# Kernel tuning notes

Measured on AMD Instinct MI355X. Metric: run time of the kernel, lower is better.

## Reference

```python
import jax, jax.numpy as jnp
import numpy as np

T = 2048
HIDDEN = 4096
NQ = 32
NKV = 8
HD = 128
THETA = 10000.0


def setup_inputs() -> dict:
    key = jax.random.key(0)
    ks = jax.random.split(key, 5)
    s = 1.0 / np.sqrt(HIDDEN)
    return {
        "positions": jnp.arange(T, dtype=jnp.int32),
        "hidden_states": jax.random.normal(ks[0], (T, HIDDEN), dtype=jnp.float32),
        "wq": jax.random.normal(ks[1], (HIDDEN, NQ * HD), dtype=jnp.float32) * s,
        "wk": jax.random.normal(ks[2], (HIDDEN, NKV * HD), dtype=jnp.float32) * s,
        "wv": jax.random.normal(ks[3], (HIDDEN, NKV * HD), dtype=jnp.float32) * s,
        "wo": jax.random.normal(ks[4], (NQ * HD, HIDDEN), dtype=jnp.float32) * s,
    }


def _rope_neox(x, positions):
    # x: [T, H, HD]; neox style: split halves, rotate
    half = HD // 2
    inv_freq = 1.0 / (THETA ** (jnp.arange(0, half, dtype=jnp.float32) / half))
    ang = positions.astype(jnp.float32)[:, None] * inv_freq[None, :]  # [T, half]
    cos = jnp.cos(ang)[:, None, :]  # [T, 1, half]
    sin = jnp.sin(ang)[:, None, :]
    x1, x2 = x[..., :half], x[..., half:]
    return jnp.concatenate([x1 * cos - x2 * sin, x2 * cos + x1 * sin], axis=-1)


def reference(positions, hidden_states, wq, wk, wv, wo):
    scale = HD ** -0.5
    q = (hidden_states @ wq).reshape(T, NQ, HD)
    k = (hidden_states @ wk).reshape(T, NKV, HD)
    v = (hidden_states @ wv).reshape(T, NKV, HD)
    q = _rope_neox(q, positions)
    k = _rope_neox(k, positions)
    # GQA: repeat kv heads to match q heads
    group = NQ // NKV
    k_r = jnp.repeat(k, group, axis=1)  # [T, NQ, HD]
    v_r = jnp.repeat(v, group, axis=1)
    scores = jnp.einsum('qhd,khd->hqk', q, k_r) * scale  # [NQ, T, T]
    causal = positions[:, None] >= positions[None, :]  # [T, T]
    scores = jnp.where(causal[None, :, :], scores, -jnp.inf)
    probs = jax.nn.softmax(scores, axis=-1)
    attn = jnp.einsum('hqk,khd->qhd', probs, v_r).reshape(T, NQ * HD)
    return attn @ wo
```

## Files before the change

kernel.cpp:

```cpp
#include <hip/hip_runtime.h>

#define T_SEQ  2048
#define HID    4096
#define NQH    32
#define NKVH   8
#define HDIM   128

typedef float  f32x4  __attribute__((ext_vector_type(4)));
typedef __bf16 bf16x8 __attribute__((ext_vector_type(8)));
typedef __bf16 bf16x4 __attribute__((ext_vector_type(4)));

__device__ __forceinline__ float bf2f(unsigned short u) {
  union { unsigned int i; float f; } v; v.i = ((unsigned int)u) << 16; return v.f;
}
__device__ __forceinline__ unsigned short f2bf(float f) {
  union { float f; unsigned int i; } v; v.f = f;
  unsigned int r = v.i + 0x7fffu + ((v.i >> 16) & 1u);
  return (unsigned short)(r >> 16);
}

__device__ __forceinline__ f32x4 mfma_bf16(bf16x8 a, bf16x8 b, f32x4 c) {
  return __builtin_amdgcn_mfma_f32_16x16x32_bf16(a, b, c, 0, 0, 0);
}

#define GLOAD16(g, l)                                              \
  __builtin_amdgcn_global_load_lds(                                \
      (const __attribute__((address_space(1))) void*)(g),          \
      (__attribute__((address_space(3))) void*)(l), 16, 0, 0)

__global__ void prep_qw(const float* __restrict__ hs, unsigned short* __restrict__ hb,
                        const float* __restrict__ wq, unsigned short* __restrict__ wt) {
  __shared__ float tile[64][65];
  if (blockIdx.x < 8192) {
    long long i = ((long long)blockIdx.x * 256 + threadIdx.x) * 4;
    float4 v = *(const float4*)(hs + i);
    union { unsigned short u[4]; uint2 p; } o;
    o.u[0] = f2bf(v.x); o.u[1] = f2bf(v.y); o.u[2] = f2bf(v.z); o.u[3] = f2bf(v.w);
    *(uint2*)(hb + i) = o.p;
    return;
  }
  const int bid = blockIdx.x - 8192;
  const int N = NQH * HDIM, K = HID;
  int n0 = (bid & 63) * 64, k0 = (bid >> 6) * 64;
  int tx = threadIdx.x & 15, ty = threadIdx.x >> 4;
#pragma unroll
  for (int i = 0; i < 4; i++) {
    int k = ty + 16 * i;
    float4 f = *(const float4*)(wq + (long long)(k0 + k) * N + n0 + tx * 4);
    tile[tx * 4 + 0][k] = f.x;
    tile[tx * 4 + 1][k] = f.y;
    tile[tx * 4 + 2][k] = f.z;
    tile[tx * 4 + 3][k] = f.w;
  }
  __syncthreads();
#pragma unroll
  for (int i = 0; i < 4; i++) {
    int n = ty + 16 * i;
    union { unsigned short u[4]; uint2 p; } o;
    o.u[0] = f2bf(tile[n][tx * 4 + 0]);
    o.u[1] = f2bf(tile[n][tx * 4 + 1]);
    o.u[2] = f2bf(tile[n][tx * 4 + 2]);
    o.u[3] = f2bf(tile[n][tx * 4 + 3]);
    *(uint2*)(wt + (long long)(n0 + n) * K + k0 + tx * 4) = o.p;
  }
}

__global__ void transpose_conv(const float* __restrict__ W,
                               unsigned short* __restrict__ Wt, int K, int N) {
  __shared__ float tile[64][65];
  int n0 = blockIdx.x * 64, k0 = blockIdx.y * 64;
  int tx = threadIdx.x & 15, ty = threadIdx.x >> 4;
#pragma unroll
  for (int i = 0; i < 4; i++) {
    int k = ty + 16 * i;
    float4 f = *(const float4*)(W + (long long)(k0 + k) * N + n0 + tx * 4);
    tile[tx * 4 + 0][k] = f.x;
    tile[tx * 4 + 1][k] = f.y;
    tile[tx * 4 + 2][k] = f.z;
    tile[tx * 4 + 3][k] = f.w;
  }
  __syncthreads();
#pragma unroll
  for (int i = 0; i < 4; i++) {
    int n = ty + 16 * i;
    union { unsigned short u[4]; uint2 p; } o;
    o.u[0] = f2bf(tile[n][tx * 4 + 0]);
    o.u[1] = f2bf(tile[n][tx * 4 + 1]);
    o.u[2] = f2bf(tile[n][tx * 4 + 2]);
    o.u[3] = f2bf(tile[n][tx * 4 + 3]);
    *(uint2*)(Wt + (long long)(n0 + n) * K + k0 + tx * 4) = o.p;
  }
}

__global__ void transpose_conv_kv(const float* __restrict__ Wk,
                                  const float* __restrict__ Wv,
                                  unsigned short* __restrict__ Wt) {
  __shared__ float tile[64][65];
  const int N = NKVH * HDIM, K = HID;
  const float* W = blockIdx.z ? Wv : Wk;
  unsigned short* dst = Wt + (size_t)blockIdx.z * N * K;
  int n0 = blockIdx.x * 64, k0 = blockIdx.y * 64;
  int tx = threadIdx.x & 15, ty = threadIdx.x >> 4;
#pragma unroll
  for (int i = 0; i < 4; i++) {
    int k = ty + 16 * i;
    float4 f = *(const float4*)(W + (long long)(k0 + k) * N + n0 + tx * 4);
    tile[tx * 4 + 0][k] = f.x;
    tile[tx * 4 + 1][k] = f.y;
    tile[tx * 4 + 2][k] = f.z;
    tile[tx * 4 + 3][k] = f.w;
  }
  __syncthreads();
#pragma unroll
  for (int i = 0; i < 4; i++) {
    int n = ty + 16 * i;
    union { unsigned short u[4]; uint2 p; } o;
    o.u[0] = f2bf(tile[n][tx * 4 + 0]);
    o.u[1] = f2bf(tile[n][tx * 4 + 1]);
    o.u[2] = f2bf(tile[n][tx * 4 + 2]);
    o.u[3] = f2bf(tile[n][tx * 4 + 3]);
    *(uint2*)(dst + (long long)(n0 + n) * K + k0 + tx * 4) = o.p;
  }
}

template <int EPI>
__global__ __launch_bounds__(256) void gemm_bt(const unsigned short* __restrict__ A,
                                               const unsigned short* __restrict__ Bt,
                                               void* __restrict__ Cv,
                                               int M, int N, int K) {
  __shared__ unsigned short As[128 * 64];
  __shared__ unsigned short Bs[128 * 64];
  const int lin = blockIdx.y * gridDim.x + blockIdx.x;
  const int cpx = (gridDim.x * gridDim.y) >> 3;
  const int swz = (lin & 7) * cpx + (lin >> 3);
  const int bx = swz % gridDim.x, by = swz / gridDim.x;

  const int t = threadIdx.x;
  const int lane = t & 63, w = t >> 6;
  const int wr = w >> 1, wc = w & 1;
  const int l15 = lane & 15, lg = lane >> 4;
  const int m0 = by * 128, n0 = bx * 128;

  f32x4 acc[4][4];
#pragma unroll
  for (int i = 0; i < 4; i++)
#pragma unroll
    for (int j = 0; j < 4; j++) acc[i][j] = (f32x4){0.f, 0.f, 0.f, 0.f};

  for (int kt = 0; kt < K; kt += 64) {
    __syncthreads();
#pragma unroll
    for (int s = 0; s < 4; s++) {
      int c = t + s * 256;
      int row = c >> 3, sub = c & 7;
      GLOAD16(A + (long long)(m0 + row) * K + kt + ((sub ^ (row & 7)) * 8),
              (char*)As + (w * 64 + s * 256) * 16);
      GLOAD16(Bt + (long long)(n0 + row) * K + kt + ((sub ^ (row & 7)) * 8),
              (char*)Bs + (w * 64 + s * 256) * 16);
    }
    __syncthreads();

#pragma unroll
    for (int kk = 0; kk < 2; kk++) {
      bf16x8 af[4], bfr[4];
#pragma unroll
      for (int mi = 0; mi < 4; mi++) {
        int row = wr * 64 + mi * 16 + l15;
        af[mi] = *(const bf16x8*)(As + row * 64 + (((kk * 4 + lg) ^ (row & 7)) * 8));
      }
#pragma unroll
      for (int ni = 0; ni < 4; ni++) {
        int row = wc * 64 + ni * 16 + l15;
        bfr[ni] = *(const bf16x8*)(Bs + row * 64 + (((kk * 4 + lg) ^ (row & 7)) * 8));
      }
#pragma unroll
      for (int mi = 0; mi < 4; mi++)
#pragma unroll
        for (int ni = 0; ni < 4; ni++)
          acc[mi][ni] = mfma_bf16(af[mi], bfr[ni], acc[mi][ni]);
    }
  }

  const int row0 = m0 + wr * 64, col0 = n0 + wc * 64;
#pragma unroll
  for (int mi = 0; mi < 4; mi++)
#pragma unroll
    for (int ni = 0; ni < 4; ni++) {
      int rbase = row0 + mi * 16 + lg * 4;
      int col = col0 + ni * 16 + l15;
#pragma unroll
      for (int r = 0; r < 4; r++) {
        float v = acc[mi][ni][r];
        if (EPI == 0)
          ((unsigned short*)Cv)[(long long)(rbase + r) * N + col] = f2bf(v);
        else
          ((float*)Cv)[(long long)(rbase + r) * N + col] = v;
      }
    }
}

__global__ __launch_bounds__(256) void gemm_kv64(const unsigned short* __restrict__ A,
                                                 const unsigned short* __restrict__ Bt,
                                                 unsigned short* __restrict__ Ckv,
                                                 unsigned short* __restrict__ Cvt) {
  __shared__ unsigned short As[64 * 64];
  __shared__ unsigned short Bs[128 * 64];
  __shared__ unsigned short Tt[128 * 64];
  const int lin = blockIdx.y * gridDim.x + blockIdx.x;
  const int swz = (lin & 7) * 64 + (lin >> 3);
  const int bx = swz & 15, by = swz >> 4;

  const int t = threadIdx.x;
  const int lane = t & 63, w = t >> 6;
  const int wr = w >> 1, wc = w & 1;
  const int l15 = lane & 15, lg = lane >> 4;
  const int m0 = by * 64, n0 = bx * 128;
  const int K = HID;

  f32x4 acc[2][4];
#pragma unroll
  for (int i = 0; i < 2; i++)
#pragma unroll
    for (int j = 0; j < 4; j++) acc[i][j] = (f32x4){0.f, 0.f, 0.f, 0.f};

  for (int kt = 0; kt < K; kt += 64) {
    __syncthreads();
#pragma unroll
    for (int s = 0; s < 2; s++) {
      int c = t + s * 256;
      int row = c >> 3, sub = c & 7;
      GLOAD16(A + (long long)(m0 + row) * K + kt + ((sub ^ (row & 7)) * 8),
              (char*)As + (w * 64 + s * 256) * 16);
    }
#pragma unroll
    for (int s = 0; s < 4; s++) {
      int c = t + s * 256;
      int row = c >> 3, sub = c & 7;
      GLOAD16(Bt + (long long)(n0 + row) * K + kt + ((sub ^ (row & 7)) * 8),
              (char*)Bs + (w * 64 + s * 256) * 16);
    }
    __syncthreads();

#pragma unroll
    for (int kk = 0; kk < 2; kk++) {
      bf16x8 af[2], bfr[4];
#pragma unroll
      for (int mi = 0; mi < 2; mi++) {
        int row = wr * 32 + mi * 16 + l15;
        af[mi] = *(const bf16x8*)(As + row * 64 + (((kk * 4 + lg) ^ (row & 7)) * 8));
      }
#pragma unroll
      for (int ni = 0; ni < 4; ni++) {
        int row = wc * 64 + ni * 16 + l15;
        bfr[ni] = *(const bf16x8*)(Bs + row * 64 + (((kk * 4 + lg) ^ (row & 7)) * 8));
      }
#pragma unroll
      for (int mi = 0; mi < 2; mi++)
#pragma unroll
        for (int ni = 0; ni < 4; ni++)
          acc[mi][ni] = mfma_bf16(af[mi], bfr[ni], acc[mi][ni]);
    }
  }

  const int row0 = m0 + wr * 32, col0 = n0 + wc * 64;
  if (n0 < 1024) {
#pragma unroll
    for (int mi = 0; mi < 2; mi++)
#pragma unroll
      for (int ni = 0; ni < 4; ni++) {
        int rbase = row0 + mi * 16 + lg * 4;
        int col = col0 + ni * 16 + l15;
#pragma unroll
        for (int r = 0; r < 4; r++)
          Ckv[(long long)(rbase + r) * 1024 + col] = f2bf(acc[mi][ni][r]);
      }
  } else {
#pragma unroll
    for (int mi = 0; mi < 2; mi++)
#pragma unroll
      for (int ni = 0; ni < 4; ni++) {
        int nloc = wc * 64 + ni * 16 + l15;
#pragma unroll
        for (int r = 0; r < 4; r++) {
          int mloc = wr * 32 + mi * 16 + lg * 4 + r;
          Tt[nloc * 64 + (mloc ^ ((nloc & 7) << 3))] = f2bf(acc[mi][ni][r]);
        }
      }
    __syncthreads();
    const int nloc = t >> 1;
#pragma unroll
    for (int cc = 0; cc < 4; cc++) {
      int ci = (t & 1) * 4 + cc;
      int sc = ci ^ (nloc & 7);
      uint4 v = *(const uint4*)(Tt + nloc * 64 + sc * 8);
      *(uint4*)(Cvt + (long long)(n0 - 1024 + nloc) * T_SEQ + m0 + ci * 8) = v;
    }
  }
}

__global__ void rope_all(unsigned short* __restrict__ qb,
                         unsigned short* __restrict__ kb,
                         const int* __restrict__ positions) {
  const int w = threadIdx.x >> 6, d = threadIdx.x & 63;
  const int gid = blockIdx.x * 4 + w;
  unsigned short* row;
  int t;
  bool isq;
  if (gid < T_SEQ * NQH) {
    int h = gid & (NQH - 1); t = gid >> 5;
    row = qb + (size_t)t * (NQH * HDIM) + (size_t)h * HDIM;
    isq = true;
  } else {
    int g = gid - T_SEQ * NQH;
    int h = g & (NKVH - 1); t = g >> 3;
    row = kb + (size_t)t * (NKVH * HDIM) + (size_t)h * HDIM;
    isq = false;
  }
  double inv = exp2(-(double)d * 0.20762050593046014);
  double ang = (double)positions[t] * inv;
  double c = cos(ang), s = sin(ang);
  if (isq) { c *= 0.12751744416986895; s *= 0.12751744416986895; }
  float x1 = bf2f(row[d]), x2 = bf2f(row[d + 64]);
  row[d]      = f2bf((float)((double)x1 * c - (double)x2 * s));
  row[d + 64] = f2bf((float)((double)x2 * c + (double)x1 * s));
}

__global__ __launch_bounds__(256) void attn_kernel(const unsigned short* __restrict__ qb,
                                                   const unsigned short* __restrict__ kb,
                                                   const unsigned short* __restrict__ vt,
                                                   unsigned short* __restrict__ ab) {
  __shared__ unsigned short Ks[64 * 128];
  __shared__ unsigned short Vs[128 * 64];

  const int lin = blockIdx.y * gridDim.x + blockIdx.x;
  const int swz = (lin & 7) * 128 + (lin >> 3);
  const int bx = swz & 63;
  const int hp = swz >> 6;
  const int kvh = hp >> 1;
  const int t = threadIdx.x, lane = t & 63, w = t >> 6;
  const int l15 = lane & 15, lg = lane >> 4;
  const int head = 2 * hp + (w & 1);
  const int wr16 = (w >> 1) * 16;
  const int jt = (hp & 1) ? bx : 63 - bx;
  const int q0 = jt * 32;

  bf16x8 qf[4];
#pragma unroll
  for (int kk = 0; kk < 4; kk++)
    qf[kk] = *(const bf16x8*)(qb + (long long)(q0 + wr16 + l15) * (NQH * HDIM) +
                              head * HDIM + kk * 32 + lg * 8);

  f32x4 accO[8];
#pragma unroll
  for (int db = 0; db < 8; db++) accO[db] = (f32x4){0.f, 0.f, 0.f, 0.f};
  float mrun = -3e38f, lrun = 0.f;

  const int jd = jt >> 1;
  for (int kt = 0; kt <= jd; kt++) {
    __syncthreads();
#pragma unroll
    for (int s = 0; s < 4; s++) {
      int c = t + s * 256;
      int row = c >> 4, chk = c & 15;
      GLOAD16(kb + (long long)(kt * 64 + row) * (NKVH * HDIM) + kvh * HDIM +
                  ((chk ^ (row & 7)) * 8),
              (char*)Ks + (w * 64 + s * 256) * 16);
    }
#pragma unroll
    for (int s = 0; s < 4; s++) {
      int c = t + s * 256;
      int row = c >> 3, chk = c & 7;
      GLOAD16(vt + (long long)(kvh * HDIM + row) * T_SEQ + kt * 64 +
                  ((chk ^ (row & 7)) * 8),
              (char*)Vs + (w * 64 + s * 256) * 16);
    }
    __syncthreads();

    f32x4 accS[4];
#pragma unroll
    for (int kc = 0; kc < 4; kc++) accS[kc] = (f32x4){0.f, 0.f, 0.f, 0.f};
    __builtin_amdgcn_s_setprio(1);
#pragma unroll
    for (int kk = 0; kk < 4; kk++)
#pragma unroll
      for (int kc = 0; kc < 4; kc++) {
        int row = kc * 16 + l15;
        bf16x8 a = *(const bf16x8*)(Ks + row * 128 + (((kk * 4 + lg) ^ (l15 & 7)) * 8));
        accS[kc] = mfma_bf16(a, qf[kk], accS[kc]);
      }
    __builtin_amdgcn_s_setprio(0);

    float pm[4][4];
    if (kt == jd) {
      const int qloc = (jt & 1) * 32 + wr16 + l15;
#pragma unroll
      for (int kc = 0; kc < 4; kc++)
#pragma unroll
        for (int r = 0; r < 4; r++)
          pm[kc][r] = (kc * 16 + lg * 4 + r > qloc) ? -3e38f : accS[kc][r];
    } else {
#pragma unroll
      for (int kc = 0; kc < 4; kc++)
#pragma unroll
        for (int r = 0; r < 4; r++) pm[kc][r] = accS[kc][r];
    }

    float rm = pm[0][0];
#pragma unroll
    for (int kc = 0; kc < 4; kc++)
#pragma unroll
      for (int r = 0; r < 4; r++) rm = fmaxf(rm, pm[kc][r]);
    if (__any(rm > mrun + 8.f)) {
      rm = fmaxf(rm, __shfl_xor(rm, 16, 64));
      rm = fmaxf(rm, __shfl_xor(rm, 32, 64));
      float mn = fmaxf(mrun, rm);
      float corr = exp2f(mrun - mn);
      mrun = mn;
      lrun *= corr;
      float cO[4];
#pragma unroll
      for (int r = 0; r < 4; r++) cO[r] = __shfl(corr, lg * 4 + r, 64);
#pragma unroll
      for (int db = 0; db < 8; db++)
#pragma unroll
        for (int r = 0; r < 4; r++) accO[db][r] *= cO[r];
    }

    float p[4][4];
#pragma unroll
    for (int kc = 0; kc < 4; kc++)
#pragma unroll
      for (int r = 0; r < 4; r++) {
        p[kc][r] = exp2f(pm[kc][r] - mrun);
        lrun += p[kc][r];
      }
    bf16x8 pa0, pa1;
#pragma unroll
    for (int j = 0; j < 8; j++) {
      pa0[j] = (__bf16)p[(j >> 2)][j & 3];
      pa1[j] = (__bf16)p[2 + (j >> 2)][j & 3];
    }

    const int swl = l15 & 7;
    const int coff = (lg & 1) * 4;
    const int c80 = lg >> 1;
    __builtin_amdgcn_s_setprio(1);
#pragma unroll
    for (int db = 0; db < 8; db++) {
      int vb = (db * 16 + l15) * 64;
      union { bf16x8 v; bf16x4 h[2]; } b;
      b.h[0] = *(const bf16x4*)(Vs + vb + ((c80 ^ swl) * 8 + coff));
      b.h[1] = *(const bf16x4*)(Vs + vb + (((c80 + 2) ^ swl) * 8 + coff));
      accO[db] = mfma_bf16(pa0, b.v, accO[db]);
    }
#pragma unroll
    for (int db = 0; db < 8; db++) {
      int vb = (db * 16 + l15) * 64;
      union { bf16x8 v; bf16x4 h[2]; } b;
      b.h[0] = *(const bf16x4*)(Vs + vb + (((c80 + 4) ^ swl) * 8 + coff));
      b.h[1] = *(const bf16x4*)(Vs + vb + (((c80 + 6) ^ swl) * 8 + coff));
      accO[db] = mfma_bf16(pa1, b.v, accO[db]);
    }
    __builtin_amdgcn_s_setprio(0);
  }

  lrun += __shfl_xor(lrun, 16, 64);
  lrun += __shfl_xor(lrun, 32, 64);
  float lO[4];
#pragma unroll
  for (int r = 0; r < 4; r++) lO[r] = __shfl(lrun, lg * 4 + r, 64);
#pragma unroll
  for (int db = 0; db < 8; db++)
#pragma unroll
    for (int r = 0; r < 4; r++) {
      int qr = q0 + wr16 + lg * 4 + r;
      int col = head * HDIM + db * 16 + l15;
      ((__bf16*)ab)[(long long)qr * (NQH * HDIM) + col] = (__bf16)(accO[db][r] / lO[r]);
    }
}

extern "C" void kernel_launch(void* const* d_in, const int* in_sizes, int n_in,
                              void* d_out, int out_size, void* d_ws, size_t ws_size,
                              hipStream_t stream) {
  const int*   positions = (const int*)d_in[0];
  const float* hs = (const float*)d_in[1];
  const float* wq = (const float*)d_in[2];
  const float* wk = (const float*)d_in[3];
  const float* wv = (const float*)d_in[4];
  const float* wo = (const float*)d_in[5];
  float* out = (float*)d_out;

  const size_t SZ_WT = (size_t)HID * HID * 2;
  const size_t SZ_HB = (size_t)T_SEQ * HID * 2;
  const size_t SZ_QB = (size_t)T_SEQ * NQH * HDIM * 2;
  const size_t SZ_KB = (size_t)T_SEQ * NKVH * HDIM * 2;
  const size_t need = SZ_WT + SZ_HB + SZ_QB + SZ_KB * 2;
  if (ws_size < need) return;

  char* p = (char*)d_ws;
  unsigned short* wt  = (unsigned short*)p; p += SZ_WT;
  unsigned short* hb  = (unsigned short*)p; p += SZ_HB;
  unsigned short* qb  = (unsigned short*)p; p += SZ_QB;
  unsigned short* kb  = (unsigned short*)p; p += SZ_KB;
  unsigned short* vtb = (unsigned short*)p; p += SZ_KB;
  unsigned short* ab  = hb;

  prep_qw<<<8192 + 4096, 256, 0, stream>>>(hs, hb, wq, wt);
  gemm_bt<0><<<dim3((NQH * HDIM) / 128, T_SEQ / 128), 256, 0, stream>>>(hb, wt, qb, T_SEQ, NQH * HDIM, HID);

  transpose_conv_kv<<<dim3((NKVH * HDIM) / 64, HID / 64, 2), 256, 0, stream>>>(wk, wv, wt);
  gemm_kv64<<<dim3(16, 32), 256, 0, stream>>>(hb, wt, kb, vtb);

  rope_all<<<(T_SEQ * (NQH + NKVH)) / 4, 256, 0, stream>>>(qb, kb, positions);

  attn_kernel<<<dim3(64, 16), 256, 0, stream>>>(qb, kb, vtb, ab);

  transpose_conv<<<dim3(HID / 64, (NQH * HDIM) / 64), 256, 0, stream>>>(wo, wt, NQH * HDIM, HID);
  gemm_bt<2><<<dim3(HID / 128, T_SEQ / 128), 256, 0, stream>>>(ab, wt, out, T_SEQ, HID, NQH * HDIM);
}
```

Measured before the change: 390.5 us.

## Make attention a persistent kernel with per-XCD atomic work queues

Replaces the fixed 64x16 attention grid with 512 persistent blocks. Each block pulls work items (one head, one 64-row query tile) from a per-XCD atomic counter, which rope_all resets. Items are handed out longest-first and each XCD is pinned to one KV head, to improve load balance and L2 reuse of K/V. The V^T store in gemm_kv64 is reordered so the attention kernel can read V fragments as single 16-byte LDS loads instead of two 8-byte halves. The risks are atomic overhead, a dependence on round-robin mapping of blocks to XCDs, and fewer blocks in flight.

```diff
diff --git a/kernel.cpp b/kernel.cpp
--- a/kernel.cpp
+++ b/kernel.cpp
@@ -8,7 +8,6 @@
 
 typedef float  f32x4  __attribute__((ext_vector_type(4)));
 typedef __bf16 bf16x8 __attribute__((ext_vector_type(8)));
-typedef __bf16 bf16x4 __attribute__((ext_vector_type(4)));
 
 __device__ __forceinline__ float bf2f(unsigned short u) {
   union { unsigned int i; float f; } v; v.i = ((unsigned int)u) << 16; return v.f;
@@ -289,18 +288,21 @@
     __syncthreads();
     const int nloc = t >> 1;
 #pragma unroll
-    for (int cc = 0; cc < 4; cc++) {
-      int ci = (t & 1) * 4 + cc;
-      int sc = ci ^ (nloc & 7);
-      uint4 v = *(const uint4*)(Tt + nloc * 64 + sc * 8);
-      *(uint4*)(Cvt + (long long)(n0 - 1024 + nloc) * T_SEQ + m0 + ci * 8) = v;
+    for (int cc = 0; cc < 8; cc++) {
+      int ci = (t & 1) * 8 + cc;
+      uint2 v = *(const uint2*)(Tt + nloc * 64 +
+                                (((ci >> 1) ^ (nloc & 7)) * 8 + (ci & 1) * 4));
+      int nc = (ci >> 3) * 8 + 2 * (ci & 3) + ((ci >> 2) & 1);
+      *(uint2*)(Cvt + (long long)(n0 - 1024 + nloc) * T_SEQ + m0 + nc * 4) = v;
     }
   }
 }
 
 __global__ void rope_all(unsigned short* __restrict__ qb,
                          unsigned short* __restrict__ kb,
-                         const int* __restrict__ positions) {
+                         const int* __restrict__ positions,
+                         int* __restrict__ cnt) {
+  if (blockIdx.x == 0 && threadIdx.x < 8) cnt[threadIdx.x] = 0;
   const int w = threadIdx.x >> 6, d = threadIdx.x & 63;
   const int gid = blockIdx.x * 4 + w;
   unsigned short* row;
@@ -328,155 +330,153 @@
 __global__ __launch_bounds__(256) void attn_kernel(const unsigned short* __restrict__ qb,
                                                    const unsigned short* __restrict__ kb,
                                                    const unsigned short* __restrict__ vt,
-                                                   unsigned short* __restrict__ ab) {
+                                                   unsigned short* __restrict__ ab,
+                                                   int* __restrict__ cnt) {
   __shared__ unsigned short Ks[64 * 128];
   __shared__ unsigned short Vs[128 * 64];
-
-  const int lin = blockIdx.y * gridDim.x + blockIdx.x;
-  const int swz = (lin & 7) * 128 + (lin >> 3);
-  const int bx = swz & 63;
-  const int hp = swz >> 6;
-  const int kvh = hp >> 1;
+  __shared__ int s_item;
+
+  const int xcd = blockIdx.x & 7;
+  const int kvh = xcd;
   const int t = threadIdx.x, lane = t & 63, w = t >> 6;
   const int l15 = lane & 15, lg = lane >> 4;
-  const int head = 2 * hp + (w & 1);
-  const int wr16 = (w >> 1) * 16;
-  const int jt = (hp & 1) ? bx : 63 - bx;
-  const int q0 = jt * 32;
-
-  bf16x8 qf[4];
-#pragma unroll
-  for (int kk = 0; kk < 4; kk++)
-    qf[kk] = *(const bf16x8*)(qb + (long long)(q0 + wr16 + l15) * (NQH * HDIM) +
-                              head * HDIM + kk * 32 + lg * 8);
-
-  f32x4 accO[8];
-#pragma unroll
-  for (int db = 0; db < 8; db++) accO[db] = (f32x4){0.f, 0.f, 0.f, 0.f};
-  float mrun = -3e38f, lrun = 0.f;
-
-  const int jd = jt >> 1;
-  for (int kt = 0; kt <= jd; kt++) {
-    __syncthreads();
-#pragma unroll
-    for (int s = 0; s < 4; s++) {
-      int c = t + s * 256;
-      int row = c >> 4, chk = c & 15;
-      GLOAD16(kb + (long long)(kt * 64 + row) * (NKVH * HDIM) + kvh * HDIM +
-                  ((chk ^ (row & 7)) * 8),
-              (char*)Ks + (w * 64 + s * 256) * 16);
-    }
-#pragma unroll
-    for (int s = 0; s < 4; s++) {
-      int c = t + s * 256;
-      int row = c >> 3, chk = c & 7;
-      GLOAD16(vt + (long long)(kvh * HDIM + row) * T_SEQ + kt * 64 +
-                  ((chk ^ (row & 7)) * 8),
-              (char*)Vs + (w * 64 + s * 256) * 16);
-    }
-    __syncthreads();
-
-    f32x4 accS[4];
-#pragma unroll
-    for (int kc = 0; kc < 4; kc++) accS[kc] = (f32x4){0.f, 0.f, 0.f, 0.f};
-    __builtin_amdgcn_s_setprio(1);
+
+  for (;;) {
+    __syncthreads();
+    if (t == 0) s_item = atomicAdd(&cnt[xcd], 1);
+    __syncthreads();
+    const int item = s_item;
+    if (item >= 128) break;
+    const int j = 31 - (item >> 2);
+    const int head = xcd * 4 + (item & 3);
+    const int q0 = j * 64;
+
+    bf16x8 qf[4];
 #pragma unroll
     for (int kk = 0; kk < 4; kk++)
-#pragma unroll
-      for (int kc = 0; kc < 4; kc++) {
-        int row = kc * 16 + l15;
-        bf16x8 a = *(const bf16x8*)(Ks + row * 128 + (((kk * 4 + lg) ^ (l15 & 7)) * 8));
-        accS[kc] = mfma_bf16(a, qf[kk], accS[kc]);
-      }
-    __builtin_amdgcn_s_setprio(0);
-
-    float pm[4][4];
-    if (kt == jd) {
-      const int qloc = (jt & 1) * 32 + wr16 + l15;
+      qf[kk] = *(const bf16x8*)(qb + (long long)(q0 + w * 16 + l15) * (NQH * HDIM) +
+                                head * HDIM + kk * 32 + lg * 8);
+
+    f32x4 accO[8];
+#pragma unroll
+    for (int db = 0; db < 8; db++) accO[db] = (f32x4){0.f, 0.f, 0.f, 0.f};
+    float mrun = -3e38f, lrun = 0.f;
+
+    for (int kt = 0; kt <= j; kt++) {
+      __syncthreads();
+#pragma unroll
+      for (int s = 0; s < 4; s++) {
+        int c = t + s * 256;
+        int row = c >> 4, chk = c & 15;
+        GLOAD16(kb + (long long)(kt * 64 + row) * (NKVH * HDIM) + kvh * HDIM +
+                    ((chk ^ (row & 7)) * 8),
+                (char*)Ks + (w * 64 + s * 256) * 16);
+      }
+#pragma unroll
+      for (int s = 0; s < 4; s++) {
+        int c = t + s * 256;
+        int row = c >> 3, chk = c & 7;
+        GLOAD16(vt + (long long)(kvh * HDIM + row) * T_SEQ + kt * 64 +
+                    ((chk ^ (row & 7)) * 8),
+                (char*)Vs + (w * 64 + s * 256) * 16);
+      }
+      __syncthreads();
+
+      f32x4 accS[4];
+#pragma unroll
+      for (int kc = 0; kc < 4; kc++) accS[kc] = (f32x4){0.f, 0.f, 0.f, 0.f};
+      __builtin_amdgcn_s_setprio(1);
+#pragma unroll
+      for (int kk = 0; kk < 4; kk++)
+#pragma unroll
+        for (int kc = 0; kc < 4; kc++) {
+          int row = kc * 16 + l15;
+          bf16x8 a = *(const bf16x8*)(Ks + row * 128 + (((kk * 4 + lg) ^ (l15 & 7)) * 8));
+          accS[kc] = mfma_bf16(a, qf[kk], accS[kc]);
+        }
+      __builtin_amdgcn_s_setprio(0);
+
+      float pm[4][4];
+      if (kt == j) {
+        const int qloc = w * 16 + l15;
+#pragma unroll
+        for (int kc = 0; kc < 4; kc++)
+#pragma unroll
+          for (int r = 0; r < 4; r++)
+            pm[kc][r] = (kc * 16 + lg * 4 + r > qloc) ? -3e38f : accS[kc][r];
+      } else {
+#pragma unroll
+        for (int kc = 0; kc < 4; kc++)
+#pragma unroll
+          for (int r = 0; r < 4; r++) pm[kc][r] = accS[kc][r];
+      }
+
+      float rm = pm[0][0];
 #pragma unroll
       for (int kc = 0; kc < 4; kc++)
 #pragma unroll
-        for (int r = 0; r < 4; r++)
-          pm[kc][r] = (kc * 16 + lg * 4 + r > qloc) ? -3e38f : accS[kc][r];
-    } else {
+        for (int r = 0; r < 4; r++) rm = fmaxf(rm, pm[kc][r]);
+      if (__any(rm > mrun + 8.f)) {
+        rm = fmaxf(rm, __shfl_xor(rm, 16, 64));
+        rm = fmaxf(rm, __shfl_xor(rm, 32, 64));
+        float mn = fmaxf(mrun, rm);
+        float corr = exp2f(mrun - mn);
+        mrun = mn;
+        lrun *= corr;
+        float cO[4];
+#pragma unroll
+        for (int r = 0; r < 4; r++) cO[r] = __shfl(corr, lg * 4 + r, 64);
+#pragma unroll
+        for (int db = 0; db < 8; db++)
+#pragma unroll
+          for (int r = 0; r < 4; r++) accO[db][r] *= cO[r];
+      }
+
+      float p[4][4];
 #pragma unroll
       for (int kc = 0; kc < 4; kc++)
 #pragma unroll
-        for (int r = 0; r < 4; r++) pm[kc][r] = accS[kc][r];
-    }
-
-    float rm = pm[0][0];
-#pragma unroll
-    for (int kc = 0; kc < 4; kc++)
-#pragma unroll
-      for (int r = 0; r < 4; r++) rm = fmaxf(rm, pm[kc][r]);
-    if (__any(rm > mrun + 8.f)) {
-      rm = fmaxf(rm, __shfl_xor(rm, 16, 64));
-      rm = fmaxf(rm, __shfl_xor(rm, 32, 64));
-      float mn = fmaxf(mrun, rm);
-      float corr = exp2f(mrun - mn);
-      mrun = mn;
-      lrun *= corr;
-      float cO[4];
-#pragma unroll
-      for (int r = 0; r < 4; r++) cO[r] = __shfl(corr, lg * 4 + r, 64);
-#pragma unroll
-      for (int db = 0; db < 8; db++)
-#pragma unroll
-        for (int r = 0; r < 4; r++) accO[db][r] *= cO[r];
-    }
-
-    float p[4][4];
-#pragma unroll
-    for (int kc = 0; kc < 4; kc++)
+        for (int r = 0; r < 4; r++) {
+          p[kc][r] = exp2f(pm[kc][r] - mrun);
+          lrun += p[kc][r];
+        }
+      bf16x8 pa0, pa1;
+#pragma unroll
+      for (int jj = 0; jj < 8; jj++) {
+        pa0[jj] = (__bf16)p[(jj >> 2)][jj & 3];
+        pa1[jj] = (__bf16)p[2 + (jj >> 2)][jj & 3];
+      }
+
+      __builtin_amdgcn_s_setprio(1);
+#pragma unroll
+      for (int db = 0; db < 8; db++) {
+        int vrow = db * 16 + l15;
+        bf16x8 b = *(const bf16x8*)(Vs + vrow * 64 + ((lg ^ (vrow & 7)) * 8));
+        accO[db] = mfma_bf16(pa0, b, accO[db]);
+      }
+#pragma unroll
+      for (int db = 0; db < 8; db++) {
+        int vrow = db * 16 + l15;
+        bf16x8 b = *(const bf16x8*)(Vs + vrow * 64 + (((4 + lg) ^ (vrow & 7)) * 8));
+        accO[db] = mfma_bf16(pa1, b, accO[db]);
+      }
+      __builtin_amdgcn_s_setprio(0);
+    }
+
+    lrun += __shfl_xor(lrun, 16, 64);
+    lrun += __shfl_xor(lrun, 32, 64);
+    float lO[4];
+#pragma unroll
+    for (int r = 0; r < 4; r++) lO[r] = __shfl(lrun, lg * 4 + r, 64);
+#pragma unroll
+    for (int db = 0; db < 8; db++)
 #pragma unroll
       for (int r = 0; r < 4; r++) {
-        p[kc][r] = exp2f(pm[kc][r] - mrun);
-        lrun += p[kc][r];
-      }
-    bf16x8 pa0, pa1;
-#pragma unroll
-    for (int j = 0; j < 8; j++) {
-      pa0[j] = (__bf16)p[(j >> 2)][j & 3];
-      pa1[j] = (__bf16)p[2 + (j >> 2)][j & 3];
-    }
-
-    const int swl = l15 & 7;
-    const int coff = (lg & 1) * 4;
-    const int c80 = lg >> 1;
-    __builtin_amdgcn_s_setprio(1);
-#pragma unroll
-    for (int db = 0; db < 8; db++) {
-      int vb = (db * 16 + l15) * 64;
-      union { bf16x8 v; bf16x4 h[2]; } b;
-      b.h[0] = *(const bf16x4*)(Vs + vb + ((c80 ^ swl) * 8 + coff));
-      b.h[1] = *(const bf16x4*)(Vs + vb + (((c80 + 2) ^ swl) * 8 + coff));
-      accO[db] = mfma_bf16(pa0, b.v, accO[db]);
-    }
-#pragma unroll
-    for (int db = 0; db < 8; db++) {
-      int vb = (db * 16 + l15) * 64;
-      union { bf16x8 v; bf16x4 h[2]; } b;
-      b.h[0] = *(const bf16x4*)(Vs + vb + (((c80 + 4) ^ swl) * 8 + coff));
-      b.h[1] = *(const bf16x4*)(Vs + vb + (((c80 + 6) ^ swl) * 8 + coff));
-      accO[db] = mfma_bf16(pa1, b.v, accO[db]);
-    }
-    __builtin_amdgcn_s_setprio(0);
-  }
-
-  lrun += __shfl_xor(lrun, 16, 64);
-  lrun += __shfl_xor(lrun, 32, 64);
-  float lO[4];
-#pragma unroll
-  for (int r = 0; r < 4; r++) lO[r] = __shfl(lrun, lg * 4 + r, 64);
-#pragma unroll
-  for (int db = 0; db < 8; db++)
-#pragma unroll
-    for (int r = 0; r < 4; r++) {
-      int qr = q0 + wr16 + lg * 4 + r;
-      int col = head * HDIM + db * 16 + l15;
-      ((__bf16*)ab)[(long long)qr * (NQH * HDIM) + col] = (__bf16)(accO[db][r] / lO[r]);
-    }
+        int qr = q0 + w * 16 + lg * 4 + r;
+        int col = head * HDIM + db * 16 + l15;
+        ((__bf16*)ab)[(long long)qr * (NQH * HDIM) + col] = (__bf16)(accO[db][r] / lO[r]);
+      }
+  }
 }
 
 extern "C" void kernel_launch(void* const* d_in, const int* in_sizes, int n_in,
@@ -494,7 +494,7 @@
   const size_t SZ_HB = (size_t)T_SEQ * HID * 2;
   const size_t SZ_QB = (size_t)T_SEQ * NQH * HDIM * 2;
   const size_t SZ_KB = (size_t)T_SEQ * NKVH * HDIM * 2;
-  const size_t need = SZ_WT + SZ_HB + SZ_QB + SZ_KB * 2;
+  const size_t need = SZ_WT + SZ_HB + SZ_QB + SZ_KB * 2 + 64;
   if (ws_size < need) return;
 
   char* p = (char*)d_ws;
@@ -503,6 +503,7 @@
   unsigned short* qb  = (unsigned short*)p; p += SZ_QB;
   unsigned short* kb  = (unsigned short*)p; p += SZ_KB;
   unsigned short* vtb = (unsigned short*)p; p += SZ_KB;
+  int* cnt = (int*)p;
   unsigned short* ab  = hb;
 
   prep_qw<<<8192 + 4096, 256, 0, stream>>>(hs, hb, wq, wt);
@@ -511,9 +512,9 @@
   transpose_conv_kv<<<dim3((NKVH * HDIM) / 64, HID / 64, 2), 256, 0, stream>>>(wk, wv, wt);
   gemm_kv64<<<dim3(16, 32), 256, 0, stream>>>(hb, wt, kb, vtb);
 
-  rope_all<<<(T_SEQ * (NQH + NKVH)) / 4, 256, 0, stream>>>(qb, kb, positions);
-
-  attn_kernel<<<dim3(64, 16), 256, 0, stream>>>(qb, kb, vtb, ab);
+  rope_all<<<(T_SEQ * (NQH + NKVH)) / 4, 256, 0, stream>>>(qb, kb, positions, cnt);
+
+  attn_kernel<<<512, 256, 0, stream>>>(qb, kb, vtb, ab, cnt);
 
   transpose_conv<<<dim3(HID / 64, (NQH * HDIM) / 64), 256, 0, stream>>>(wo, wt, NQH * HDIM, HID);
   gemm_bt<2><<<dim3(HID / 128, T_SEQ / 128), 256, 0, stream>>>(ab, wt, out, T_SEQ, HID, NQH * HDIM);
```

Measured after the change: 358.9 us. 8.1% less time.
